# Kernel tuning notes

Hardware: AMD Instinct MI355X
Metric: run time of the kernel (lower is better)

## Reference

```python
import jax, jax.numpy as jnp
import numpy as np

DT = 0.01
DAMP_MIN = 5e-4


def setup_inputs() -> dict:
    key = jax.random.key(0)
    ks = jax.random.split(key, 6)
    B_batch, L, Din, N = 4, 4096, 512, 256
    u = jax.random.normal(ks[0], (B_batch, L, Din), dtype=jnp.float32)
    # parameters, initialized as in the torch module
    A_real = jax.random.normal(ks[1], (N,), dtype=jnp.float32) * 0.1 - DAMP_MIN
    A_imag = jax.random.normal(ks[2], (N,), dtype=jnp.float32)
    B_mat = jax.random.normal(ks[3], (N, Din), dtype=jnp.float32) * 0.02
    C_mat = jax.random.normal(ks[4], (Din, N), dtype=jnp.float32) * 0.02
    D_vec = jax.random.normal(ks[5], (Din,), dtype=jnp.float32)
    return {"u": u, "A_real": A_real, "A_imag": A_imag,
            "B_mat": B_mat, "C_mat": C_mat, "D_vec": D_vec}


def reference(u, A_real, A_imag, B_mat, C_mat, D_vec):
    L = u.shape[1]
    # bilinear (Tustin) discretization of diagonal A
    a_real = -jnp.abs(A_real) - DAMP_MIN
    A = jax.lax.complex(a_real, A_imag)                      # [N]
    denom = 1.0 - (DT * 0.5) * A
    A_bar = (1.0 + (DT * 0.5) * A) / denom                   # [N]
    B_bar = DT * B_mat.astype(jnp.complex64) / denom[:, None]  # [N, Din]
    # convolution kernel via explicit powers: K[n, t] = A_bar[n]^t
    k = jnp.arange(L, dtype=jnp.float32)
    A_pow = A_bar[:, None] ** k[None, :]                     # [N, L]
    # project input into state space: v[b, t, n]
    v = jnp.einsum('bld,nd->bln', u.astype(jnp.complex64), B_bar)
    # FFT convolution, zero-padded to 2L (linear convolution)
    n_fft = 2 * L
    v_f = jnp.fft.fft(v, n=n_fft, axis=1)                    # [B, 2L, N]
    k_f = jnp.fft.fft(A_pow.T, n=n_fft, axis=0)              # [2L, N]
    y = jnp.fft.ifft(v_f * k_f[None, :, :], axis=1)[:, :L, :]  # [B, L, N]
    # output projection + skip path
    y_out = jnp.einsum('bln,dn->bld', y, C_mat.astype(jnp.complex64)).real
    return y_out + u * D_vec
```

## Files before the change

kernel.cpp:

```cpp
#include <hip/hip_runtime.h>

#define L_SEQ 4096
#define DIN   512
#define NST   256

typedef __attribute__((ext_vector_type(8))) short short8;
typedef __attribute__((ext_vector_type(4))) float f32x4;

__device__ inline unsigned short f2bf(float f) {
  unsigned u = __builtin_bit_cast(unsigned, f);
  unsigned r = (u + 0x7FFFu + ((u >> 16) & 1u)) >> 16;
  return (unsigned short)r;
}
__device__ inline float bf2f(unsigned short h) {
  unsigned u = ((unsigned)h) << 16;
  return __builtin_bit_cast(float, u);
}

__global__ __launch_bounds__(256) void prep_kernel(
    const float* __restrict__ A_real, const float* __restrict__ A_imag,
    const float* __restrict__ B_mat, const float* __restrict__ C_mat,
    float* __restrict__ abr, float* __restrict__ abi,
    unsigned short* __restrict__ bmbf, unsigned short* __restrict__ cbf) {
  const int n = blockIdx.x;
  const float ar = -fabsf(A_real[n]) - 5e-4f;
  const float ai = A_imag[n];
  const float dr = 1.0f - 0.005f * ar;
  const float di = -0.005f * ai;
  const float inv = 1.0f / (dr * dr + di * di);
  if (threadIdx.x == 0) {
    const float nr = 1.0f + 0.005f * ar;
    const float ni = 0.005f * ai;
    abr[n] = (nr * dr + ni * di) * inv;
    abi[n] = (ni * dr - nr * di) * inv;
  }
  const float cr = 0.01f * dr * inv;
  const float ci = -0.01f * di * inv;
  for (int d = threadIdx.x; d < DIN; d += blockDim.x) {
    const float bv = B_mat[n * DIN + d];
    bmbf[n * DIN + d]         = f2bf(bv * cr);
    bmbf[(NST + n) * DIN + d] = f2bf(bv * ci);
  }
  const size_t cbase = (size_t)(2 * n) * NST;
  for (int k = threadIdx.x; k < 2 * NST; k += blockDim.x)
    cbf[cbase + k] = f2bf(C_mat[cbase + k]);
}

__global__ __launch_bounds__(256, 2) void gemm1_mfma(
    const float* __restrict__ U,
    const unsigned short* __restrict__ Bmbf,
    unsigned short* __restrict__ V) {
  __shared__ short At[2][128 * 32];
  __shared__ short Bt[2][128 * 32];
  const int tid  = threadIdx.x;
  const int wave = tid >> 6;
  const int lane = tid & 63;
  const int m0 = blockIdx.x * 128;
  const int j0 = blockIdx.y * 128;

  f32x4 acc[4][4];
#pragma unroll
  for (int i = 0; i < 4; ++i)
#pragma unroll
    for (int j = 0; j < 4; ++j) acc[i][j] = (f32x4)0.f;

  const int wr = wave >> 1, wc = wave & 1;
  const int cl = lane & 15;
  const int kq = lane >> 4;

  const int arow = tid >> 1;
  const int acol = (tid & 1) * 16;
  const float* gA = U + (size_t)(m0 + arow) * 512 + acol;

  f32x4 areg[4];
#define LOADA(k0)                                                               \
  {                                                                             \
    _Pragma("unroll")                                                           \
    for (int q = 0; q < 4; ++q)                                                 \
      areg[q] = *reinterpret_cast<const f32x4*>(gA + (k0) + q * 4);             \
  }
#define WRITEA(buf)                                                             \
  {                                                                             \
    unsigned short o16[16];                                                     \
    _Pragma("unroll")                                                           \
    for (int q = 0; q < 4; ++q) {                                               \
      o16[q * 4 + 0] = f2bf(areg[q].x); o16[q * 4 + 1] = f2bf(areg[q].y);       \
      o16[q * 4 + 2] = f2bf(areg[q].z); o16[q * 4 + 3] = f2bf(areg[q].w);       \
    }                                                                           \
    short* dst = &At[buf][arow * 32 + acol];                                    \
    *reinterpret_cast<short8*>(dst)     = *reinterpret_cast<short8*>(&o16[0]);  \
    *reinterpret_cast<short8*>(dst + 8) = *reinterpret_cast<short8*>(&o16[8]);  \
  }
#define STAGEB(buf, k0)                                                         \
  {                                                                             \
    _Pragma("unroll")                                                           \
    for (int q = 0; q < 2; ++q) {                                               \
      const int row = wave * 32 + q * 16 + (lane >> 2);                         \
      const int kb  = lane & 3;                                                 \
      const unsigned short* gB = Bmbf + (size_t)(j0 + row) * 512 + (k0) + kb*8; \
      short* lB = &Bt[buf][(wave * 32 + q * 16) * 32];                          \
      __builtin_amdgcn_global_load_lds(                                         \
          (const __attribute__((address_space(1))) void*)gB,                    \
          (__attribute__((address_space(3))) void*)lB, 16, 0, 0);               \
    }                                                                           \
  }

  LOADA(0)
  STAGEB(0, 0)
  for (int s = 0; s < 16; ++s) {
    const int cur = s & 1;
    WRITEA(cur)
    if (s < 15) {
      LOADA((s + 1) * 32)
      STAGEB(cur ^ 1, (s + 1) * 32)
    }
    __syncthreads();
    short8 a[4], b[4];
#pragma unroll
    for (int f = 0; f < 4; ++f) {
      a[f] = *reinterpret_cast<const short8*>(&At[cur][(wr * 64 + f * 16 + cl) * 32 + kq * 8]);
      b[f] = *reinterpret_cast<const short8*>(&Bt[cur][(wc * 64 + f * 16 + cl) * 32 + kq * 8]);
    }
#pragma unroll
    for (int fm = 0; fm < 4; ++fm)
#pragma unroll
      for (int fn = 0; fn < 4; ++fn)
        acc[fm][fn] = __builtin_amdgcn_mfma_f32_16x16x32_bf16(a[fm], b[fn], acc[fm][fn], 0, 0, 0);
    __syncthreads();
  }
#undef LOADA
#undef WRITEA
#undef STAGEB

  const int bb    = m0 >> 12;
  const int lbase = (m0 & 4095);
#pragma unroll
  for (int fm = 0; fm < 4; ++fm)
#pragma unroll
    for (int fn = 0; fn < 4; ++fn) {
      const int jj = j0 + wc * 64 + fn * 16 + cl;
      const int ll = lbase + wr * 64 + fm * 16 + kq * 4;
      const f32x4 v = acc[fm][fn];
      unsigned short o[4] = {f2bf(v.x), f2bf(v.y), f2bf(v.z), f2bf(v.w)};
      *reinterpret_cast<ushort4*>(&V[((size_t)bb * 512 + jj) * L_SEQ + ll]) =
          *reinterpret_cast<ushort4*>(o);
    }
}

__global__ __launch_bounds__(256) void scan_kernel(
    const unsigned short* __restrict__ V, const float* __restrict__ abr,
    const float* __restrict__ abi, unsigned short* __restrict__ Y) {
  const int b = blockIdx.x >> 8;
  const int n = blockIdx.x & 255;
  const float ar = abr[n], ai = abi[n];
  const unsigned short* vre = V + ((size_t)b * 512 + n) * L_SEQ;
  const unsigned short* vim = V + ((size_t)b * 512 + NST + n) * L_SEQ;
  const int t = threadIdx.x;
  const int lane = t & 63;
  const int wid  = t >> 6;

  float xr[16], xi[16];
#pragma unroll
  for (int q = 0; q < 2; ++q) {
    const short8 r8 = *reinterpret_cast<const short8*>(&vre[t * 16 + q * 8]);
    const short8 i8 = *reinterpret_cast<const short8*>(&vim[t * 16 + q * 8]);
#pragma unroll
    for (int j = 0; j < 8; ++j) {
      xr[q * 8 + j] = bf2f((unsigned short)r8[j]);
      xi[q * 8 + j] = bf2f((unsigned short)i8[j]);
    }
  }
  float yr = 0.f, yi = 0.f;
#pragma unroll
  for (int i = 0; i < 16; ++i) {
    const float t1 = ar * yr - ai * yi + xr[i];
    yi = ar * yi + ai * yr + xi[i];
    yr = t1;
    xr[i] = yr; xi[i] = yi;
  }
  float fr = ar, fi = ai;
#pragma unroll
  for (int s = 0; s < 4; ++s) { const float t2 = fr * fr - fi * fi; fi = 2.f * fr * fi; fr = t2; }

  float er = yr, ei = yi;
  float Fr = fr, Fi = fi;
  float Fkr[6], Fki[6];
#pragma unroll
  for (int s = 0; s < 6; ++s) {
    Fkr[s] = Fr; Fki[s] = Fi;
    const float pr = __shfl_up(er, 1 << s);
    const float pi = __shfl_up(ei, 1 << s);
    if (lane >= (1 << s)) {
      er += Fr * pr - Fi * pi;
      ei += Fr * pi + Fi * pr;
    }
    const float t2 = Fr * Fr - Fi * Fi; Fi = 2.f * Fr * Fi; Fr = t2;
  }

  __shared__ float twr[4], twi[4];
  if (lane == 63) { twr[wid] = er; twi[wid] = ei; }
  __syncthreads();
  float cwr = 0.f, cwi = 0.f;
  for (int w = 0; w < wid; ++w) {
    const float t2 = Fr * cwr - Fi * cwi + twr[w];
    cwi = Fr * cwi + Fi * cwr + twi[w];
    cwr = t2;
  }
  float sxr = __shfl_up(er, 1);
  float sxi = __shfl_up(ei, 1);
  if (lane == 0) { sxr = 0.f; sxi = 0.f; }
  float plr = 1.f, pli = 0.f;
#pragma unroll
  for (int s = 0; s < 6; ++s) {
    if (lane & (1 << s)) {
      const float t2 = plr * Fkr[s] - pli * Fki[s];
      pli = plr * Fki[s] + pli * Fkr[s];
      plr = t2;
    }
  }
  float cr = sxr + plr * cwr - pli * cwi;
  float ci = sxi + plr * cwi + pli * cwr;

  unsigned short o16[16];
  float gr = cr, gi = ci;
#pragma unroll
  for (int i = 0; i < 16; ++i) {
    const float t1 = ar * gr - ai * gi;
    gi = ar * gi + ai * gr;
    gr = t1;
    o16[i] = f2bf(xr[i] + gr);
  }
  unsigned short* yo = Y + ((size_t)b * NST + n) * L_SEQ + t * 16;
  *reinterpret_cast<short8*>(&yo[0]) = *reinterpret_cast<short8*>(&o16[0]);
  *reinterpret_cast<short8*>(&yo[8]) = *reinterpret_cast<short8*>(&o16[8]);
}

__global__ __launch_bounds__(256) void transp_kernel(
    const unsigned short* __restrict__ Y, unsigned short* __restrict__ Yt) {
  __shared__ unsigned short T[64 * 256];
  const int b  = blockIdx.z;
  const int n0 = blockIdx.y * 64;
  const int l0 = blockIdx.x * 256;
  const int t  = threadIdx.x;
  {
    const int nr = t >> 2;
    const int c4 = t & 3;
    const unsigned short* src = Y + ((size_t)b * NST + n0 + nr) * L_SEQ + l0;
#pragma unroll
    for (int h = 0; h < 8; ++h) {
      const int ch = c4 + h * 4;
      const short8 v = *reinterpret_cast<const short8*>(&src[ch * 8]);
      const int p = ch ^ (nr & 7) ^ ((nr >> 3) & 3);
      *reinterpret_cast<short8*>(&T[nr * 256 + p * 8]) = v;
    }
  }
  __syncthreads();
  {
    const int c = t & 7;
#pragma unroll
    for (int h2 = 0; h2 < 8; ++h2) {
      const int l = h2 * 32 + (t >> 3);
      unsigned short o[8];
#pragma unroll
      for (int j = 0; j < 8; ++j) {
        const int p = (l >> 3) ^ j ^ (c & 3);
        o[j] = T[(c * 8 + j) * 256 + p * 8 + (l & 7)];
      }
      *reinterpret_cast<short8*>(&Yt[((size_t)b * L_SEQ + l0 + l) * NST + n0 + c * 8]) =
          *reinterpret_cast<short8*>(o);
    }
  }
}

__global__ __launch_bounds__(256, 2) void gemm2_mfma(
    const unsigned short* __restrict__ Cbf,
    const unsigned short* __restrict__ Yt,
    const float* __restrict__ U,
    const float* __restrict__ Dv,
    float* __restrict__ out) {
  __shared__ short At[2][128 * 32];
  __shared__ short Bt[2][128 * 32];
  const int tid  = threadIdx.x;
  const int wave = tid >> 6;
  const int lane = tid & 63;
  const int m0 = blockIdx.x * 128;
  const int d0 = blockIdx.y * 128;

  f32x4 acc[4][4];
#pragma unroll
  for (int i = 0; i < 4; ++i)
#pragma unroll
    for (int j = 0; j < 4; ++j) acc[i][j] = (f32x4)0.f;

  const int wr = wave >> 1, wc = wave & 1;
  const int cl = lane & 15;
  const int kq = lane >> 4;

#define STAGE2(buf, k0)                                                         \
  {                                                                             \
    _Pragma("unroll")                                                           \
    for (int q = 0; q < 2; ++q) {                                               \
      const int row = wave * 32 + q * 16 + (lane >> 2);                         \
      const int kb  = lane & 3;                                                 \
      const unsigned short* gA = Cbf + (size_t)(d0 + row) * 256 + (k0) + kb*8;  \
      const unsigned short* gB = Yt  + (size_t)(m0 + row) * 256 + (k0) + kb*8;  \
      short* lA = &At[buf][(wave * 32 + q * 16) * 32];                          \
      short* lB = &Bt[buf][(wave * 32 + q * 16) * 32];                          \
      __builtin_amdgcn_global_load_lds(                                         \
          (const __attribute__((address_space(1))) void*)gA,                    \
          (__attribute__((address_space(3))) void*)lA, 16, 0, 0);               \
      __builtin_amdgcn_global_load_lds(                                         \
          (const __attribute__((address_space(1))) void*)gB,                    \
          (__attribute__((address_space(3))) void*)lB, 16, 0, 0);               \
    }                                                                           \
  }

  STAGE2(0, 0)
  for (int s = 0; s < 8; ++s) {
    const int cur = s & 1;
    if (s < 7) STAGE2(cur ^ 1, (s + 1) * 32)
    __syncthreads();
    short8 a[4], b[4];
#pragma unroll
    for (int f = 0; f < 4; ++f) {
      a[f] = *reinterpret_cast<const short8*>(&At[cur][(wr * 64 + f * 16 + cl) * 32 + kq * 8]);
      b[f] = *reinterpret_cast<const short8*>(&Bt[cur][(wc * 64 + f * 16 + cl) * 32 + kq * 8]);
    }
#pragma unroll
    for (int fm = 0; fm < 4; ++fm)
#pragma unroll
      for (int fn = 0; fn < 4; ++fn)
        acc[fm][fn] = __builtin_amdgcn_mfma_f32_16x16x32_bf16(a[fm], b[fn], acc[fm][fn], 0, 0, 0);
    __syncthreads();
  }
#undef STAGE2

#pragma unroll
  for (int fm = 0; fm < 4; ++fm) {
    const int dd = d0 + wr * 64 + fm * 16 + kq * 4;
    const f32x4 dvv = *reinterpret_cast<const f32x4*>(&Dv[dd]);
#pragma unroll
    for (int fn = 0; fn < 4; ++fn) {
      const size_t ll = m0 + wc * 64 + fn * 16 + cl;
      const size_t base = ll * 512 + dd;
      const f32x4 uv = *reinterpret_cast<const f32x4*>(&U[base]);
      f32x4 o = acc[fm][fn];
      o.x += uv.x * dvv.x; o.y += uv.y * dvv.y;
      o.z += uv.z * dvv.z; o.w += uv.w * dvv.w;
      *reinterpret_cast<f32x4*>(&out[base]) = o;
    }
  }
}

extern "C" void kernel_launch(void* const* d_in, const int* in_sizes, int n_in,
                              void* d_out, int out_size, void* d_ws, size_t ws_size,
                              hipStream_t stream) {
  const float* u      = (const float*)d_in[0];
  const float* A_real = (const float*)d_in[1];
  const float* A_imag = (const float*)d_in[2];
  const float* B_mat  = (const float*)d_in[3];
  const float* C_mat  = (const float*)d_in[4];
  const float* D_vec  = (const float*)d_in[5];
  float* out = (float*)d_out;

  unsigned short* bmbf = (unsigned short*)d_ws;
  unsigned short* cbf  = bmbf + 512 * 512;
  float* abr = (float*)(cbf + 512 * 256);
  float* abi = abr + 256;
  unsigned short* V   = (unsigned short*)(abi + 256);
  unsigned short* Y   = V + (size_t)4 * 512 * 4096;
  unsigned short* Yt  = Y + (size_t)4 * 256 * 4096;

  hipLaunchKernelGGL(prep_kernel, dim3(NST), dim3(256), 0, stream,
                     A_real, A_imag, B_mat, C_mat, abr, abi, bmbf, cbf);
  hipLaunchKernelGGL(gemm1_mfma, dim3(128, 4), dim3(256), 0, stream, u, bmbf, V);
  hipLaunchKernelGGL(scan_kernel, dim3(1024), dim3(256), 0, stream, V, abr, abi, Y);
  hipLaunchKernelGGL(transp_kernel, dim3(16, 4, 4), dim3(256), 0, stream, Y, Yt);
  hipLaunchKernelGGL(gemm2_mfma, dim3(128, 4), dim3(256), 0, stream, cbf, Yt, u, D_vec, out);
}
```

Before: 62.19 us.

## Retile input projection GEMM to full-width 32-row tiles reading u once

The first GEMM now uses 32-row by 512-column output tiles per block instead of 128x128 tiles, so each row of u is read and converted to bf16 only once rather than four times across column blocks. The grid becomes 512 one-dimensional blocks, each wave owning 128 output columns. The double-buffered LDS pipeline is replaced by a single buffer with an extra barrier before the next B stage is loaded. This costs some overlap between loads and MFMA, and every block re-reads the full B matrix slice per k-step.

```diff
diff --git a/kernel.cpp b/kernel.cpp
--- a/kernel.cpp
+++ b/kernel.cpp
@@ -46,59 +46,48 @@
     cbf[cbase + k] = f2bf(C_mat[cbase + k]);
 }
 
-__global__ __launch_bounds__(256, 2) void gemm1_mfma(
+__global__ __launch_bounds__(256, 2) void gemm1_full(
     const float* __restrict__ U,
     const unsigned short* __restrict__ Bmbf,
     unsigned short* __restrict__ V) {
-  __shared__ short At[2][128 * 32];
-  __shared__ short Bt[2][128 * 32];
+  __shared__ short At[32 * 32];
+  __shared__ short Bt[512 * 32];
   const int tid  = threadIdx.x;
   const int wave = tid >> 6;
   const int lane = tid & 63;
-  const int m0 = blockIdx.x * 128;
-  const int j0 = blockIdx.y * 128;
-
-  f32x4 acc[4][4];
-#pragma unroll
-  for (int i = 0; i < 4; ++i)
-#pragma unroll
-    for (int j = 0; j < 4; ++j) acc[i][j] = (f32x4)0.f;
-
-  const int wr = wave >> 1, wc = wave & 1;
+  const int mb = blockIdx.x;
+  const int m0 = mb * 32;
+
+  f32x4 acc[2][8];
+#pragma unroll
+  for (int i = 0; i < 2; ++i)
+#pragma unroll
+    for (int j = 0; j < 8; ++j) acc[i][j] = (f32x4)0.f;
+
   const int cl = lane & 15;
   const int kq = lane >> 4;
 
-  const int arow = tid >> 1;
-  const int acol = (tid & 1) * 16;
+  const int arow = tid >> 3;
+  const int acol = (tid & 7) * 4;
   const float* gA = U + (size_t)(m0 + arow) * 512 + acol;
-
-  f32x4 areg[4];
-#define LOADA(k0)                                                               \
+  float4 areg;
+
+#define LOADA(k0)  { areg = *reinterpret_cast<const float4*>(gA + (k0)); }
+#define WRITEA()                                                                \
+  {                                                                             \
+    unsigned short o4[4] = {f2bf(areg.x), f2bf(areg.y), f2bf(areg.z),           \
+                            f2bf(areg.w)};                                      \
+    *reinterpret_cast<ushort4*>(&At[arow * 32 + acol]) =                        \
+        *reinterpret_cast<ushort4*>(o4);                                        \
+  }
+#define STAGEB(k0)                                                              \
   {                                                                             \
     _Pragma("unroll")                                                           \
-    for (int q = 0; q < 4; ++q)                                                 \
-      areg[q] = *reinterpret_cast<const f32x4*>(gA + (k0) + q * 4);             \
-  }
-#define WRITEA(buf)                                                             \
-  {                                                                             \
-    unsigned short o16[16];                                                     \
-    _Pragma("unroll")                                                           \
-    for (int q = 0; q < 4; ++q) {                                               \
-      o16[q * 4 + 0] = f2bf(areg[q].x); o16[q * 4 + 1] = f2bf(areg[q].y);       \
-      o16[q * 4 + 2] = f2bf(areg[q].z); o16[q * 4 + 3] = f2bf(areg[q].w);       \
-    }                                                                           \
-    short* dst = &At[buf][arow * 32 + acol];                                    \
-    *reinterpret_cast<short8*>(dst)     = *reinterpret_cast<short8*>(&o16[0]);  \
-    *reinterpret_cast<short8*>(dst + 8) = *reinterpret_cast<short8*>(&o16[8]);  \
-  }
-#define STAGEB(buf, k0)                                                         \
-  {                                                                             \
-    _Pragma("unroll")                                                           \
-    for (int q = 0; q < 2; ++q) {                                               \
-      const int row = wave * 32 + q * 16 + (lane >> 2);                         \
-      const int kb  = lane & 3;                                                 \
-      const unsigned short* gB = Bmbf + (size_t)(j0 + row) * 512 + (k0) + kb*8; \
-      short* lB = &Bt[buf][(wave * 32 + q * 16) * 32];                          \
+    for (int q = 0; q < 8; ++q) {                                               \
+      const int rowbase = wave * 128 + q * 16;                                  \
+      const unsigned short* gB =                                                \
+          Bmbf + (size_t)(rowbase + (lane >> 2)) * 512 + (k0) + (lane & 3) * 8; \
+      short* lB = &Bt[rowbase * 32];                                            \
       __builtin_amdgcn_global_load_lds(                                         \
           (const __attribute__((address_space(1))) void*)gB,                    \
           (__attribute__((address_space(3))) void*)lB, 16, 0, 0);               \
@@ -106,40 +95,41 @@
   }
 
   LOADA(0)
-  STAGEB(0, 0)
+  STAGEB(0)
   for (int s = 0; s < 16; ++s) {
-    const int cur = s & 1;
-    WRITEA(cur)
+    WRITEA()
+    if (s < 15) LOADA((s + 1) * 32)
+    __syncthreads();
+    short8 a[2], b[8];
+#pragma unroll
+    for (int f = 0; f < 2; ++f)
+      a[f] = *reinterpret_cast<const short8*>(&At[(f * 16 + cl) * 32 + kq * 8]);
+#pragma unroll
+    for (int f = 0; f < 8; ++f)
+      b[f] = *reinterpret_cast<const short8*>(
+          &Bt[(wave * 128 + f * 16 + cl) * 32 + kq * 8]);
+#pragma unroll
+    for (int fm = 0; fm < 2; ++fm)
+#pragma unroll
+      for (int fn = 0; fn < 8; ++fn)
+        acc[fm][fn] = __builtin_amdgcn_mfma_f32_16x16x32_bf16(a[fm], b[fn], acc[fm][fn], 0, 0, 0);
     if (s < 15) {
-      LOADA((s + 1) * 32)
-      STAGEB(cur ^ 1, (s + 1) * 32)
-    }
-    __syncthreads();
-    short8 a[4], b[4];
-#pragma unroll
-    for (int f = 0; f < 4; ++f) {
-      a[f] = *reinterpret_cast<const short8*>(&At[cur][(wr * 64 + f * 16 + cl) * 32 + kq * 8]);
-      b[f] = *reinterpret_cast<const short8*>(&Bt[cur][(wc * 64 + f * 16 + cl) * 32 + kq * 8]);
-    }
-#pragma unroll
-    for (int fm = 0; fm < 4; ++fm)
-#pragma unroll
-      for (int fn = 0; fn < 4; ++fn)
-        acc[fm][fn] = __builtin_amdgcn_mfma_f32_16x16x32_bf16(a[fm], b[fn], acc[fm][fn], 0, 0, 0);
-    __syncthreads();
+      __syncthreads();
+      STAGEB((s + 1) * 32)
+    }
   }
 #undef LOADA
 #undef WRITEA
 #undef STAGEB
 
-  const int bb    = m0 >> 12;
-  const int lbase = (m0 & 4095);
-#pragma unroll
-  for (int fm = 0; fm < 4; ++fm)
-#pragma unroll
-    for (int fn = 0; fn < 4; ++fn) {
-      const int jj = j0 + wc * 64 + fn * 16 + cl;
-      const int ll = lbase + wr * 64 + fm * 16 + kq * 4;
+  const int bb    = mb >> 7;
+  const int lbase = (mb & 127) * 32;
+#pragma unroll
+  for (int fm = 0; fm < 2; ++fm)
+#pragma unroll
+    for (int fn = 0; fn < 8; ++fn) {
+      const int jj = wave * 128 + fn * 16 + cl;
+      const int ll = lbase + fm * 16 + kq * 4;
       const f32x4 v = acc[fm][fn];
       unsigned short o[4] = {f2bf(v.x), f2bf(v.y), f2bf(v.z), f2bf(v.w)};
       *reinterpret_cast<ushort4*>(&V[((size_t)bb * 512 + jj) * L_SEQ + ll]) =
@@ -373,7 +363,7 @@
 
   hipLaunchKernelGGL(prep_kernel, dim3(NST), dim3(256), 0, stream,
                      A_real, A_imag, B_mat, C_mat, abr, abi, bmbf, cbf);
-  hipLaunchKernelGGL(gemm1_mfma, dim3(128, 4), dim3(256), 0, stream, u, bmbf, V);
+  hipLaunchKernelGGL(gemm1_full, dim3(512), dim3(256), 0, stream, u, bmbf, V);
   hipLaunchKernelGGL(scan_kernel, dim3(1024), dim3(256), 0, stream, V, abr, abi, Y);
   hipLaunchKernelGGL(transp_kernel, dim3(16, 4, 4), dim3(256), 0, stream, Y, Yt);
   hipLaunchKernelGGL(gemm2_mfma, dim3(128, 4), dim3(256), 0, stream, cbf, Yt, u, D_vec, out);
```

Result: slower. 64.50 us (+3.7%).
